# Optimization experiments

Hardware: AMD Instinct MI355X
Metric: run time of the kernel (lower is better)

Reference implementation:

```python
import jax, jax.numpy as jnp
import numpy as np

K = 1000            # top-k kept per batch element
BG = 0              # background class index
B = 64              # number of batch elements (segments)
NPB = 16384         # candidates per batch element (>= K, equal segments)
C = 80              # number of classes


def setup_inputs() -> dict:
    key = jax.random.key(0)
    k1, k2 = jax.random.split(key)
    scores = jax.random.uniform(k1, (B * NPB, C), dtype=jnp.float32)
    # monotonically rising batch indices, NPB entries per batch
    batch_indices = jnp.repeat(jnp.arange(B, dtype=jnp.int32), NPB)
    boxes = jax.random.normal(k2, (B * NPB, 4), dtype=jnp.float32)
    return {"scores": scores, "batch_indices": batch_indices, "boxes": boxes}


def reference(scores, batch_indices, boxes):
    # foreground score = 1 - P(background)
    fg = 1.0 - scores[:, BG]                         # [N]
    # equal segments -> ragged per-batch top-k == batched top-k
    per_batch = fg.reshape(B, NPB)                   # [B, NPB]
    _, idx = jax.lax.top_k(per_batch, K)             # [B, K] local indices
    offsets = jnp.arange(B, dtype=idx.dtype)[:, None] * NPB
    top_indices = (idx + offsets).reshape(-1)        # [B*K] global indices
    filtered_scores = scores[top_indices]            # [B*K, C]
    filtered_batch_indices = batch_indices[top_indices]  # [B*K]
    filtered_boxes = boxes[top_indices]              # [B*K, 4]
    return (filtered_scores, filtered_batch_indices, filtered_boxes)
```

## Files before the change

### kernel.cpp

```cpp
#include <hip/hip_runtime.h>
#include <stdint.h>

#define BATCHES 64
#define NPB     16384
#define NCLS    80
#define TOPK    1000
#define NTH     1024
#define PER     (NPB / NTH)
#define SELCAP  2048
#define GROWS   16
#define GTH     320

__device__ __forceinline__ uint32_t fg_key(float s) {
    float fg = 1.0f - s;
    if (fg >= 1.0f) return 0xFFFFFFFFu;
    if (fg <= 0.0f) return 0u;
    return (uint32_t)(fg * 4294967296.0f);
}

__global__ __launch_bounds__(256) void key_kernel(const float* __restrict__ scores,
                                                  uint32_t* __restrict__ keys) {
    int gid = blockIdx.x * 256 + threadIdx.x;
    keys[gid] = fg_key(scores[(size_t)gid * NCLS]);
}

__global__ __launch_bounds__(NTH) void select_kernel(const uint32_t* __restrict__ keys,
                                                     int* __restrict__ ordidx) {
    __shared__ __align__(16) uint32_t hist[256];
    __shared__ uint32_t bc_prefix, bc_rem, selcnt;
    __shared__ __align__(16) unsigned long long sel[SELCAP];

    const int t = threadIdx.x;
    const int b = blockIdx.x;
    const int lane = t & 63;

    uint32_t kreg[PER];
    const uint32_t* kb = keys + (size_t)b * NPB;
#pragma unroll
    for (int i = 0; i < PER; ++i) kreg[i] = kb[i * NTH + t];

    if (t == 0) { bc_prefix = 0u; bc_rem = TOPK; selcnt = 0u; }
    __syncthreads();

    for (int shift = 24; shift >= 0; shift -= 8) {
        uint32_t prefix = bc_prefix;
        uint32_t rem    = bc_rem;
        if (t < 256) hist[t] = 0u;
        __syncthreads();
        uint32_t maskhi = (shift == 24) ? 0u : (0xFFFFFFFFu << (shift + 8));
#pragma unroll
        for (int i = 0; i < PER; ++i) {
            uint32_t kk = kreg[i];
            if ((kk & maskhi) == prefix) atomicAdd(&hist[(kk >> shift) & 0xFFu], 1u);
        }
        __syncthreads();
        if (t < 64) {
            uint4 v = ((const uint4*)hist)[lane];
            uint32_t s3 = v.w;
            uint32_t s2 = v.z + s3;
            uint32_t s1 = v.y + s2;
            uint32_t s0 = v.x + s1;
            uint32_t x = s0;
#pragma unroll
            for (int off = 1; off < 64; off <<= 1) {
                uint32_t y = (uint32_t)__shfl_down((int)x, off, 64);
                if (lane + off < 64) x += y;
            }
            uint32_t above = x - s0;
            uint32_t ge[4] = { s0 + above, s1 + above, s2 + above, s3 + above };
            uint32_t cnt[4] = { v.x, v.y, v.z, v.w };
#pragma unroll
            for (int i = 0; i < 4; ++i) {
                uint32_t gt = ge[i] - cnt[i];
                if (ge[i] >= rem && gt < rem) {
                    bc_prefix = prefix | ((uint32_t)(4 * lane + i) << shift);
                    bc_rem = rem - gt;
                }
            }
        }
        __syncthreads();
    }

    const uint32_t pivot = bc_prefix;

#pragma unroll
    for (int i = 0; i < PER; ++i) {
        bool p = kreg[i] >= pivot;
        unsigned long long m = __ballot(p);
        if (m) {
            int leader = __builtin_ctzll(m);
            uint32_t cnt = (uint32_t)__popcll(m);
            uint32_t base = 0;
            if (lane == leader) base = atomicAdd(&selcnt, cnt);
            base = (uint32_t)__shfl((int)base, leader, 64);
            if (p) {
                uint32_t pos = base + (uint32_t)__popcll(m & ((1ull << lane) - 1ull));
                if (pos < SELCAP) {
                    uint32_t lidx = (uint32_t)(i * NTH + t);
                    sel[pos] = ((unsigned long long)kreg[i] << 32) |
                               (unsigned long long)(~lidx);
                }
            }
        }
    }
    __syncthreads();
    uint32_t M = selcnt;
    if (M > SELCAP) M = SELCAP;
    if (t < 4 && M + t < SELCAP) sel[M + t] = 0ull;
    __syncthreads();

    const uint32_t Mp = (M + 3u) & ~3u;
    for (int e = t; e < (int)M; e += NTH) {
        unsigned long long mine = sel[e];
        uint32_t r = 0;
        for (uint32_t j = 0; j < Mp; j += 4) {
            unsigned long long a0 = sel[j], a1 = sel[j + 1];
            unsigned long long a2 = sel[j + 2], a3 = sel[j + 3];
            r += (a0 > mine) + (a1 > mine) + (a2 > mine) + (a3 > mine);
        }
        if (r < TOPK) {
            uint32_t lidx = ~((uint32_t)mine);
            ordidx[b * TOPK + (int)r] = b * NPB + (int)lidx;
        }
    }
}

__global__ __launch_bounds__(GTH) void gather_kernel(const float* __restrict__ scores,
                                                     const int* __restrict__ batch_indices,
                                                     const float* __restrict__ boxes,
                                                     const int* __restrict__ ordidx,
                                                     float* __restrict__ out) {
    const int t = threadIdx.x;
    const int r = t / 20;
    const int q = t % 20;
    const int row = blockIdx.x * GROWS + r;

    float* out_scores = out;
    float* out_bi     = out + (size_t)BATCHES * TOPK * NCLS;
    float* out_boxes  = out_bi + (size_t)BATCHES * TOPK;

    int g = ordidx[row];
    const float4* srow = (const float4*)(scores + (size_t)g * NCLS);
    float4 v = srow[q];
    ((float4*)(out_scores + (size_t)row * NCLS))[q] = v;
    if (q == 0) {
        ((float4*)out_boxes)[row] = ((const float4*)boxes)[g];
        out_bi[row] = (float)batch_indices[g];
    }
}

extern "C" void kernel_launch(void* const* d_in, const int* in_sizes, int n_in,
                              void* d_out, int out_size, void* d_ws, size_t ws_size,
                              hipStream_t stream) {
    const float* scores        = (const float*)d_in[0];
    const int*   batch_indices = (const int*)d_in[1];
    const float* boxes         = (const float*)d_in[2];
    float* out = (float*)d_out;

    const int N = BATCHES * NPB;
    uint32_t* keys = (uint32_t*)d_ws;
    int* ordidx = (int*)d_ws + N;

    key_kernel<<<N / 256, 256, 0, stream>>>(scores, keys);
    select_kernel<<<BATCHES, NTH, 0, stream>>>(keys, ordidx);
    gather_kernel<<<(BATCHES * TOPK) / GROWS, GTH, 0, stream>>>(
        scores, batch_indices, boxes, ordidx, out);
}
```

Measured before the change: 446.9 us.

## Replace multi-pass radix select with single-pass top-byte bucket scatter and per-bin ranking

Cuts the four-pass 8-bit radix select down to a single histogram over each key's top byte. Candidates whose top byte is at or above the threshold bin are then scattered into per-bin contiguous slots of shared memory. Each candidate's rank comes from its bin's base offset plus a count within that bin only, replacing the O(M^2) comparison over all selected candidates. The intent is to remove three histogram passes and most of the ranking work. In exchange, the threshold bin's whole population is kept (about 1000+64 elements with uniform data), and atomics now go per bin instead of per wave.

```diff
diff --git a/kernel.cpp b/kernel.cpp
--- a/kernel.cpp
+++ b/kernel.cpp
@@ -27,7 +27,9 @@
 __global__ __launch_bounds__(NTH) void select_kernel(const uint32_t* __restrict__ keys,
                                                      int* __restrict__ ordidx) {
     __shared__ __align__(16) uint32_t hist[256];
-    __shared__ uint32_t bc_prefix, bc_rem, selcnt;
+    __shared__ uint32_t basebin[256];
+    __shared__ uint32_t fill[256];
+    __shared__ uint32_t Wsh;
     __shared__ __align__(16) unsigned long long sel[SELCAP];
 
     const int t = threadIdx.x;
@@ -39,85 +41,62 @@
 #pragma unroll
     for (int i = 0; i < PER; ++i) kreg[i] = kb[i * NTH + t];
 
-    if (t == 0) { bc_prefix = 0u; bc_rem = TOPK; selcnt = 0u; }
+    if (t < 256) { hist[t] = 0u; fill[t] = 0u; }
     __syncthreads();
 
-    for (int shift = 24; shift >= 0; shift -= 8) {
-        uint32_t prefix = bc_prefix;
-        uint32_t rem    = bc_rem;
-        if (t < 256) hist[t] = 0u;
-        __syncthreads();
-        uint32_t maskhi = (shift == 24) ? 0u : (0xFFFFFFFFu << (shift + 8));
 #pragma unroll
-        for (int i = 0; i < PER; ++i) {
-            uint32_t kk = kreg[i];
-            if ((kk & maskhi) == prefix) atomicAdd(&hist[(kk >> shift) & 0xFFu], 1u);
+    for (int i = 0; i < PER; ++i) atomicAdd(&hist[kreg[i] >> 24], 1u);
+    __syncthreads();
+
+    if (t < 64) {
+        uint4 v = ((const uint4*)hist)[lane];
+        uint32_t s3 = v.w;
+        uint32_t s2 = v.z + s3;
+        uint32_t s1 = v.y + s2;
+        uint32_t s0 = v.x + s1;
+        uint32_t x = s0;
+#pragma unroll
+        for (int off = 1; off < 64; off <<= 1) {
+            uint32_t y = (uint32_t)__shfl_down((int)x, off, 64);
+            if (lane + off < 64) x += y;
         }
-        __syncthreads();
-        if (t < 64) {
-            uint4 v = ((const uint4*)hist)[lane];
-            uint32_t s3 = v.w;
-            uint32_t s2 = v.z + s3;
-            uint32_t s1 = v.y + s2;
-            uint32_t s0 = v.x + s1;
-            uint32_t x = s0;
+        uint32_t above = x - s0;
+        uint32_t ge[4]  = { s0 + above, s1 + above, s2 + above, s3 + above };
+        uint32_t cnt[4] = { v.x, v.y, v.z, v.w };
 #pragma unroll
-            for (int off = 1; off < 64; off <<= 1) {
-                uint32_t y = (uint32_t)__shfl_down((int)x, off, 64);
-                if (lane + off < 64) x += y;
-            }
-            uint32_t above = x - s0;
-            uint32_t ge[4] = { s0 + above, s1 + above, s2 + above, s3 + above };
-            uint32_t cnt[4] = { v.x, v.y, v.z, v.w };
-#pragma unroll
-            for (int i = 0; i < 4; ++i) {
-                uint32_t gt = ge[i] - cnt[i];
-                if (ge[i] >= rem && gt < rem) {
-                    bc_prefix = prefix | ((uint32_t)(4 * lane + i) << shift);
-                    bc_rem = rem - gt;
-                }
-            }
+        for (int i = 0; i < 4; ++i) {
+            uint32_t gt = ge[i] - cnt[i];
+            basebin[4 * lane + i] = gt;
+            if (ge[i] >= TOPK && gt < TOPK) Wsh = (uint32_t)(4 * lane + i);
         }
-        __syncthreads();
     }
-
-    const uint32_t pivot = bc_prefix;
+    __syncthreads();
+    const uint32_t W = Wsh;
 
 #pragma unroll
     for (int i = 0; i < PER; ++i) {
-        bool p = kreg[i] >= pivot;
-        unsigned long long m = __ballot(p);
-        if (m) {
-            int leader = __builtin_ctzll(m);
-            uint32_t cnt = (uint32_t)__popcll(m);
-            uint32_t base = 0;
-            if (lane == leader) base = atomicAdd(&selcnt, cnt);
-            base = (uint32_t)__shfl((int)base, leader, 64);
-            if (p) {
-                uint32_t pos = base + (uint32_t)__popcll(m & ((1ull << lane) - 1ull));
-                if (pos < SELCAP) {
-                    uint32_t lidx = (uint32_t)(i * NTH + t);
-                    sel[pos] = ((unsigned long long)kreg[i] << 32) |
-                               (unsigned long long)(~lidx);
-                }
+        uint32_t kk = kreg[i];
+        uint32_t byte = kk >> 24;
+        if (byte >= W) {
+            uint32_t pos = basebin[byte] + atomicAdd(&fill[byte], 1u);
+            if (pos < SELCAP) {
+                uint32_t lidx = (uint32_t)(i * NTH + t);
+                sel[pos] = ((unsigned long long)kk << 32) |
+                           (unsigned long long)(~lidx);
             }
         }
     }
     __syncthreads();
-    uint32_t M = selcnt;
-    if (M > SELCAP) M = SELCAP;
-    if (t < 4 && M + t < SELCAP) sel[M + t] = 0ull;
-    __syncthreads();
+    const uint32_t M = basebin[W] + hist[W];
 
-    const uint32_t Mp = (M + 3u) & ~3u;
-    for (int e = t; e < (int)M; e += NTH) {
+    for (uint32_t e = (uint32_t)t; e < M && e < SELCAP; e += NTH) {
         unsigned long long mine = sel[e];
-        uint32_t r = 0;
-        for (uint32_t j = 0; j < Mp; j += 4) {
-            unsigned long long a0 = sel[j], a1 = sel[j + 1];
-            unsigned long long a2 = sel[j + 2], a3 = sel[j + 3];
-            r += (a0 > mine) + (a1 > mine) + (a2 > mine) + (a3 > mine);
-        }
+        uint32_t bin = (uint32_t)(mine >> 56);
+        uint32_t base = basebin[bin];
+        uint32_t end = base + hist[bin];
+        if (end > SELCAP) end = SELCAP;
+        uint32_t r = base;
+        for (uint32_t j = base; j < end; ++j) r += (sel[j] > mine);
         if (r < TOPK) {
             uint32_t lidx = ~((uint32_t)mine);
             ordidx[b * TOPK + (int)r] = b * NPB + (int)lidx;
```

Result: faster. 431.4 us (-3.5%).
